# Kernel optimization log

Measured on AMD Instinct MI355X. Metric: run time of the kernel, lower is better.

The kernel has to match this reference:

```python
import jax, jax.numpy as jnp
import numpy as np

N = 50000
E = 1600000
DX = 128
DH = 128
DY = 64
NEG_SLOPE = 0.0  # in_neg_slope; LeakyReLU slope in GAT attention


def _init(key, shape, fan_in):
    return jax.random.normal(key, shape, dtype=jnp.float32) / np.sqrt(fan_in)


def setup_inputs() -> dict:
    key = jax.random.key(0)
    ks = jax.random.split(key, 12)
    node_x = jax.random.normal(ks[0], (N, DX), dtype=jnp.float32)
    edge_index = jax.random.randint(ks[1], (2, E), 0, N, dtype=jnp.int32)
    return {
        "node_x": node_x,
        "edge_index": edge_index,
        # GATConv layer 1 (DX -> DH, heads=1)
        "W1": _init(ks[2], (DX, DH), DX),
        "att_src1": _init(ks[3], (DH,), DH),
        "att_dst1": _init(ks[4], (DH,), DH),
        "b1": jnp.zeros((DH,), dtype=jnp.float32),
        # GATConv layer 2 (DH -> DH)
        "W2": _init(ks[5], (DH, DH), DH),
        "att_src2": _init(ks[6], (DH,), DH),
        "att_dst2": _init(ks[7], (DH,), DH),
        "b2": jnp.zeros((DH,), dtype=jnp.float32),
        # output Linear (DH -> DY)
        "W_out": _init(ks[8], (DH, DY), DH),
        "b_out": jnp.zeros((DY,), dtype=jnp.float32),
    }


def _gat_conv(x, src, dst, W, att_src, att_dst, bias, n):
    # h: [N, DH] transformed features
    h = x @ W
    # per-edge attention logits: a_src . h_j + a_dst . h_i
    e = (h @ att_src)[src] + (h @ att_dst)[dst]          # [E']
    e = jnp.where(e > 0, e, NEG_SLOPE * e)               # LeakyReLU
    # segment softmax over incoming edges of each destination node
    m = jax.lax.stop_gradient(jax.ops.segment_max(e, dst, num_segments=n))
    ex = jnp.exp(e - m[dst])
    denom = jax.ops.segment_sum(ex, dst, num_segments=n)
    alpha = ex / denom[dst]                              # [E']
    # scatter-add weighted source features to destinations
    out = jax.ops.segment_sum(h[src] * alpha[:, None], dst, num_segments=n)
    return out + bias


def reference(node_x, edge_index, W1, att_src1, att_dst1, b1,
              W2, att_src2, att_dst2, b2, W_out, b_out):
    n = node_x.shape[0]
    src, dst = edge_index[0], edge_index[1]
    # PyG GATConv default add_self_loops=True
    loop = jnp.arange(n, dtype=src.dtype)
    src = jnp.concatenate([src, loop])
    dst = jnp.concatenate([dst, loop])
    x1 = jax.nn.relu(_gat_conv(node_x, src, dst, W1, att_src1, att_dst1, b1, n))
    x2 = _gat_conv(x1, src, dst, W2, att_src2, att_dst2, b2, n)
    return x2 @ W_out + b_out
```

## Files before the change

### kernel.cpp

```cpp
#include <hip/hip_runtime.h>
#include <hip/hip_fp16.h>

typedef unsigned short u16;
typedef unsigned int   u32;
typedef _Float16 f16;
typedef __attribute__((ext_vector_type(8))) f16 f16x8;
typedef __attribute__((ext_vector_type(2))) f16 h2;
typedef __attribute__((ext_vector_type(4))) float f32x4;

#define NN 50000
#define EE 1600000
#define DD 128
#define DYY 64
#define NB 196
#define EPB 8192
#define GB 196
#define MAXD 160
#define NTILE 3125
#define GMM 782
#define XST 144

__device__ __forceinline__ u16 f2h(float f){
  union { f16 h; u16 u; } x; x.h = (f16)f; return x.u;
}
__device__ __forceinline__ float wave_sum(float v){
  #pragma unroll
  for (int s = 32; s; s >>= 1) v += __shfl_xor(v, s, 64);
  return v;
}

__device__ __forceinline__ void wfrag_one(const float* __restrict__ W, u16* __restrict__ Wf,
                                          int nct, int s){
  int lane = s & 63;
  int t  = (s >> 6) % nct;
  int ks = (s >> 6) / nct;
  int q = lane >> 4, n = lane & 15;
  int N = nct * 16;
  u16 tmp[8];
  #pragma unroll
  for (int j = 0; j < 8; ++j)
    tmp[j] = f2h(W[(ks * 32 + q * 8 + j) * N + t * 16 + n]);
  *(uint4*)(Wf + (size_t)s * 8) = *(const uint4*)tmp;
}

__global__ __launch_bounds__(256) void kA_prep(const int* __restrict__ dst, int* __restrict__ hist2d,
                                               const float* __restrict__ W1, const float* __restrict__ W2,
                                               const float* __restrict__ Wo,
                                               u16* __restrict__ Wf1, u16* __restrict__ Wf2,
                                               u16* __restrict__ Wfo){
  int b = blockIdx.x, tid = threadIdx.x;
  if (b < GB){
    __shared__ int hist[256];
    hist[tid] = 0;
    __syncthreads();
    int e0 = b * EPB, e1 = min(e0 + EPB, EE);
    for (int e = e0 + tid; e < e1; e += 256) atomicAdd(&hist[dst[e] >> 8], 1);
    __syncthreads();
    hist2d[b * 256 + tid] = hist[tid];
  } else if (b < 204) wfrag_one(W1, Wf1, 8, (b - 196) * 256 + tid);
  else if (b < 212)   wfrag_one(W2, Wf2, 8, (b - 204) * 256 + tid);
  else                wfrag_one(Wo, Wfo, 4, (b - 212) * 256 + tid);
}

__device__ __forceinline__ void gemm_tile(const float* __restrict__ X,
                                          const u16* __restrict__ Wf, u16* __restrict__ Hout,
                                          const float* __restrict__ as, const float* __restrict__ ad,
                                          float* __restrict__ Sv, float* __restrict__ Dv,
                                          int blk, int tid, uint4* Wl){
  const uint4* Wg = (const uint4*)Wf;
  #pragma unroll
  for (int i = 0; i < 8; ++i) Wl[tid + 256 * i] = Wg[tid + 256 * i];
  __syncthreads();
  int wv = tid >> 6, lane = tid & 63;
  int rtile = blk * 4 + wv;
  if (rtile >= NTILE) return;
  int q = lane >> 4, n = lane & 15;
  int arow = rtile * 16 + n;
  f32x4 acc[8];
  #pragma unroll
  for (int t = 0; t < 8; ++t) acc[t] = (f32x4){0.f, 0.f, 0.f, 0.f};
  union F8 { uint4 u; f16x8 v; f16 h[8]; };
  #pragma unroll
  for (int ks = 0; ks < 4; ++ks){
    int kb = ks * 32 + q * 8;
    const float* xp = X + (size_t)arow * DD + kb;
    float4 f0 = *(const float4*)xp;
    float4 f1 = *(const float4*)(xp + 4);
    F8 a;
    a.h[0] = (f16)f0.x; a.h[1] = (f16)f0.y; a.h[2] = (f16)f0.z; a.h[3] = (f16)f0.w;
    a.h[4] = (f16)f1.x; a.h[5] = (f16)f1.y; a.h[6] = (f16)f1.z; a.h[7] = (f16)f1.w;
    #pragma unroll
    for (int t = 0; t < 8; ++t){
      F8 b; b.u = Wl[(ks * 8 + t) * 64 + lane];
      acc[t] = __builtin_amdgcn_mfma_f32_16x16x32_f16(a.v, b.v, acc[t], 0, 0, 0);
    }
  }
  float ps[4] = {0, 0, 0, 0}, pd[4] = {0, 0, 0, 0};
  #pragma unroll
  for (int t = 0; t < 8; ++t){
    float a_s = as[t * 16 + n];
    float a_d = ad[t * 16 + n];
    #pragma unroll
    for (int rg = 0; rg < 4; ++rg){
      ps[rg] += acc[t][rg] * a_s;
      pd[rg] += acc[t][rg] * a_d;
    }
  }
  #pragma unroll
  for (int rg = 0; rg < 4; ++rg){
    #pragma unroll
    for (int s = 1; s < 16; s <<= 1){
      ps[rg] += __shfl_xor(ps[rg], s, 64);
      pd[rg] += __shfl_xor(pd[rg], s, 64);
    }
  }
  #pragma unroll
  for (int rg = 0; rg < 4; ++rg){
    int grow = rtile * 16 + q * 4 + rg;
    if (n == 0){ Sv[grow] = ps[rg]; Dv[grow] = pd[rg]; }
    #pragma unroll
    for (int t = 0; t < 8; ++t)
      Hout[(size_t)grow * DD + t * 16 + n] = f2h(acc[t][rg]);
  }
}

__global__ __launch_bounds__(256) void kBC(const int* __restrict__ src, const int* __restrict__ dst,
                                           const int* __restrict__ hist2d,
                                           int* __restrict__ btot, int* __restrict__ bbase,
                                           u32* __restrict__ buf,
                                           const float* __restrict__ X0, const u16* __restrict__ Wf1,
                                           u16* __restrict__ Hbf1,
                                           const float* __restrict__ as1, const float* __restrict__ ad1,
                                           float* __restrict__ Sv1, float* __restrict__ Dv1){
  __shared__ __align__(16) uint4 Wl[2048];
  int b = blockIdx.x, tid = threadIdx.x;
  if (b < GB){
    int* lcur = (int*)Wl;
    int* sd   = ((int*)Wl) + 256;
    int c = b;
    int pre = 0, tot = 0;
    for (int cc = 0; cc < GB; ++cc){
      int v = hist2d[cc * 256 + tid];
      if (cc < c) pre += v;
      tot += v;
    }
    sd[tid] = tot;
    __syncthreads();
    for (int o = 1; o < 256; o <<= 1){
      int t = (tid >= o) ? sd[tid - o] : 0;
      __syncthreads();
      sd[tid] += t;
      __syncthreads();
    }
    int bb = sd[tid] - tot;
    if (c == 0){ btot[tid] = tot; bbase[tid] = bb; }
    lcur[tid] = bb + pre;
    __syncthreads();
    int e0 = c * EPB, e1 = min(e0 + EPB, EE);
    for (int e = e0 + tid; e < e1; e += 256){
      int d = dst[e];
      int pos = atomicAdd(&lcur[d >> 8], 1);
      buf[pos] = (u32)src[e] | ((u32)(d & 255) << 16);
    }
  } else {
    gemm_tile(X0, Wf1, Hbf1, as1, ad1, Sv1, Dv1, b - GB, tid, Wl);
  }
}

__global__ __launch_bounds__(256) void kD_finalize(const u32* __restrict__ buf,
                                                   const int* __restrict__ btot, const int* __restrict__ bbase,
                                                   int* __restrict__ offs, int* __restrict__ cnt,
                                                   u16* __restrict__ srcs){
  __shared__ int dh[256];
  __shared__ int sd[256];
  __shared__ int dcur[256];
  int tid = threadIdx.x, b = blockIdx.x;
  int n = btot[b], base = bbase[b];
  dh[tid] = 0;
  __syncthreads();
  for (int i = tid; i < n; i += 256) atomicAdd(&dh[(buf[base + i] >> 16) & 255], 1);
  __syncthreads();
  int v = dh[tid];
  sd[tid] = v;
  __syncthreads();
  for (int o = 1; o < 256; o <<= 1){
    int t = (tid >= o) ? sd[tid - o] : 0;
    __syncthreads();
    sd[tid] += t;
    __syncthreads();
  }
  int excl = sd[tid] - v;
  dcur[tid] = base + excl;
  int d = (b << 8) + tid;
  if (d < NN){ offs[d] = base + excl; cnt[d] = v; }
  __syncthreads();
  for (int i = tid; i < n; i += 256){
    u32 u = buf[base + i];
    int pos = atomicAdd(&dcur[(u >> 16) & 255], 1);
    srcs[pos] = (u16)(u & 0xffffu);
  }
}

__device__ void agg_node_lds(const u16* __restrict__ H, const float* __restrict__ Sv,
                             const float* __restrict__ Dv, const int* __restrict__ offs,
                             const int* __restrict__ cnt, const u16* __restrict__ srcs,
                             const float* __restrict__ bias, u16* __restrict__ xrow,
                             int do_relu, int wid, int lane, int* si, float* sw){
  int off = offs[wid], c = cnt[wid];
  float dvw = Dv[wid];
  float wself = __expf(fmaxf(Sv[wid] + dvw, 0.f));
  int cf = min(c, MAXD);
  int grp = lane >> 4, cg_ = lane & 15;
  const u32* H32 = (const u32*)H;
  union F8 { uint4 u; h2 p[4]; };
  F8 rself; rself.u = (uint4){0, 0, 0, 0};
  if (grp == 0) rself.u = *(const uint4*)(H32 + (size_t)wid * 64 + cg_ * 4);
  float dl = 0.f;
  for (int j = lane; j < c; j += 64){
    int sidx = (int)srcs[off + j];
    float wgt = __expf(fmaxf(Sv[sidx] + dvw, 0.f));
    if (j < MAXD){ si[j] = sidx; sw[j] = wgt; }
    dl += wgt;
  }
  float inv = 1.f / (wave_sum(dl) + wself);
  h2 accA[4] = {(h2){0,0},(h2){0,0},(h2){0,0},(h2){0,0}};
  h2 accB[4] = {(h2){0,0},(h2){0,0},(h2){0,0},(h2){0,0}};
  if (grp == 0){
    f16 wh = (f16)(wself * inv); h2 w2 = {wh, wh};
    #pragma unroll
    for (int i = 0; i < 4; ++i) accA[i] = rself.p[i] * w2;
  }
  int base = 0;
  int nfull = cf & ~7;
  for (; base < nfull; base += 8){
    int j0 = base + grp, j1 = j0 + 4;
    int s0 = si[j0], s1 = si[j1];
    float w0 = sw[j0] * inv, w1 = sw[j1] * inv;
    F8 r0; r0.u = *(const uint4*)(H32 + (size_t)s0 * 64 + cg_ * 4);
    F8 r1; r1.u = *(const uint4*)(H32 + (size_t)s1 * 64 + cg_ * 4);
    f16 wh0 = (f16)w0; h2 w20 = {wh0, wh0};
    f16 wh1 = (f16)w1; h2 w21 = {wh1, wh1};
    #pragma unroll
    for (int i = 0; i < 4; ++i){
      accA[i] += r0.p[i] * w20;
      accB[i] += r1.p[i] * w21;
    }
  }
  for (; base < cf; base += 4){
    int j = base + grp;
    float wgt = 0.f; int sidx = 0;
    if (j < cf){ wgt = sw[j] * inv; sidx = si[j]; }
    f16 wh = (f16)wgt; h2 w2 = {wh, wh};
    F8 r; r.u = *(const uint4*)(H32 + (size_t)sidx * 64 + cg_ * 4);
    #pragma unroll
    for (int i = 0; i < 4; ++i) accA[i] += r.p[i] * w2;
  }
  for (int base2 = MAXD; base2 < c; base2 += 4){
    int j = base2 + grp;
    bool valid = j < c;
    int sidx = valid ? (int)srcs[off + j] : 0;
    float wgt = valid ? __expf(fmaxf(Sv[sidx] + dvw, 0.f)) * inv : 0.f;
    f16 wh = (f16)wgt; h2 w2 = {wh, wh};
    F8 r; r.u = *(const uint4*)(H32 + (size_t)sidx * 64 + cg_ * 4);
    #pragma unroll
    for (int i = 0; i < 4; ++i) accA[i] += r.p[i] * w2;
  }
  #pragma unroll
  for (int i = 0; i < 4; ++i) accA[i] += accB[i];
  union FU { h2 v; float f; };
  #pragma unroll
  for (int i = 0; i < 4; ++i){
    FU a; a.v = accA[i];
    FU o1; o1.f = __shfl_xor(a.f, 16, 64); a.v = a.v + o1.v;
    FU o2; o2.f = __shfl_xor(a.f, 32, 64); a.v = a.v + o2.v;
    accA[i] = a.v;
  }
  if (grp == 0){
    uint4 pk;
    u32* pkp = (u32*)&pk;
    #pragma unroll
    for (int qq = 0; qq < 4; ++qq){
      float o0 = (float)accA[qq].x + bias[cg_ * 8 + 2 * qq];
      float o1 = (float)accA[qq].y + bias[cg_ * 8 + 2 * qq + 1];
      if (do_relu){ o0 = fmaxf(o0, 0.f); o1 = fmaxf(o1, 0.f); }
      pkp[qq] = ((u32)f2h(o1) << 16) | (u32)f2h(o0);
    }
    *(uint4*)(xrow + cg_ * 8) = pk;
  }
}

__global__ __launch_bounds__(256, 8) void kE(const u16* __restrict__ Hbf1,
                                          const float* __restrict__ Sv1, const float* __restrict__ Dv1,
                                          const int* __restrict__ offs, const int* __restrict__ cnt,
                                          const u16* __restrict__ srcs, const float* __restrict__ b1,
                                          const u16* __restrict__ Wf2,
                                          const float* __restrict__ as2, const float* __restrict__ ad2,
                                          u16* __restrict__ Hbf2,
                                          float* __restrict__ Sv2, float* __restrict__ Dv2){
  __shared__ __align__(16) u16 Xs[16 * XST];
  __shared__ int   s_i[4][MAXD];
  __shared__ float s_w[4][MAXD];
  __shared__ float svp[16], dvp[16];
  int tid = threadIdx.x, wv = tid >> 6, lane = tid & 63;
  int rtile = blockIdx.x;
  if (tid < 16){ svp[tid] = 0.f; dvp[tid] = 0.f; }
  #pragma unroll
  for (int k = 0; k < 4; ++k){
    int r = wv * 4 + k;
    agg_node_lds(Hbf1, Sv1, Dv1, offs, cnt, srcs, b1, Xs + r * XST, 1,
                 rtile * 16 + r, lane, s_i[wv], s_w[wv]);
  }
  __syncthreads();
  const uint4* Wg = (const uint4*)Wf2;
  int q = lane >> 4, n = lane & 15;
  f32x4 acc[2] = {(f32x4){0.f,0.f,0.f,0.f}, (f32x4){0.f,0.f,0.f,0.f}};
  union F8 { uint4 u; f16x8 v; };
  #pragma unroll
  for (int ks = 0; ks < 4; ++ks){
    F8 a; a.u = *(const uint4*)((const char*)Xs + n * (XST * 2) + ks * 64 + q * 16);
    #pragma unroll
    for (int tt = 0; tt < 2; ++tt){
      F8 b; b.u = Wg[(ks * 8 + wv * 2 + tt) * 64 + lane];
      acc[tt] = __builtin_amdgcn_mfma_f32_16x16x32_f16(a.v, b.v, acc[tt], 0, 0, 0);
    }
  }
  float ps[4] = {0, 0, 0, 0}, pd[4] = {0, 0, 0, 0};
  #pragma unroll
  for (int tt = 0; tt < 2; ++tt){
    int t = wv * 2 + tt;
    float a_s = as2[t * 16 + n];
    float a_d = ad2[t * 16 + n];
    #pragma unroll
    for (int rg = 0; rg < 4; ++rg){
      ps[rg] += acc[tt][rg] * a_s;
      pd[rg] += acc[tt][rg] * a_d;
    }
  }
  #pragma unroll
  for (int rg = 0; rg < 4; ++rg){
    #pragma unroll
    for (int s = 1; s < 16; s <<= 1){
      ps[rg] += __shfl_xor(ps[rg], s, 64);
      pd[rg] += __shfl_xor(pd[rg], s, 64);
    }
  }
  if (n == 0){
    #pragma unroll
    for (int rg = 0; rg < 4; ++rg){
      atomicAdd(&svp[q * 4 + rg], ps[rg]);
      atomicAdd(&dvp[q * 4 + rg], pd[rg]);
    }
  }
  #pragma unroll
  for (int rg = 0; rg < 4; ++rg){
    int grow = rtile * 16 + q * 4 + rg;
    #pragma unroll
    for (int tt = 0; tt < 2; ++tt)
      Hbf2[(size_t)grow * DD + (wv * 2 + tt) * 16 + n] = f2h(acc[tt][rg]);
  }
  __syncthreads();
  if (tid < 16){ Sv2[rtile * 16 + tid] = svp[tid]; Dv2[rtile * 16 + tid] = dvp[tid]; }
}

__global__ __launch_bounds__(256, 8) void kF(const u16* __restrict__ Hbf2,
                                          const float* __restrict__ Sv2, const float* __restrict__ Dv2,
                                          const int* __restrict__ offs, const int* __restrict__ cnt,
                                          const u16* __restrict__ srcs, const float* __restrict__ b2,
                                          const u16* __restrict__ Wfo, const float* __restrict__ bo,
                                          float* __restrict__ out){
  __shared__ __align__(16) u16 Xs[16 * XST];
  __shared__ int   s_i[4][MAXD];
  __shared__ float s_w[4][MAXD];
  int tid = threadIdx.x, wv = tid >> 6, lane = tid & 63;
  int rtile = blockIdx.x;
  #pragma unroll
  for (int k = 0; k < 4; ++k){
    int r = wv * 4 + k;
    agg_node_lds(Hbf2, Sv2, Dv2, offs, cnt, srcs, b2, Xs + r * XST, 0,
                 rtile * 16 + r, lane, s_i[wv], s_w[wv]);
  }
  __syncthreads();
  const uint4* Wg = (const uint4*)Wfo;
  int q = lane >> 4, n = lane & 15;
  f32x4 acc = (f32x4){0.f, 0.f, 0.f, 0.f};
  union F8 { uint4 u; f16x8 v; };
  #pragma unroll
  for (int ks = 0; ks < 4; ++ks){
    F8 a; a.u = *(const uint4*)((const char*)Xs + n * (XST * 2) + ks * 64 + q * 16);
    F8 b; b.u = Wg[(ks * 4 + wv) * 64 + lane];
    acc = __builtin_amdgcn_mfma_f32_16x16x32_f16(a.v, b.v, acc, 0, 0, 0);
  }
  float bt = bo[wv * 16 + n];
  #pragma unroll
  for (int rg = 0; rg < 4; ++rg){
    int grow = rtile * 16 + q * 4 + rg;
    out[(size_t)grow * DYY + wv * 16 + n] = acc[rg] + bt;
  }
}

extern "C" void kernel_launch(void* const* d_in, const int* in_sizes, int n_in,
                              void* d_out, int out_size, void* d_ws, size_t ws_size,
                              hipStream_t stream) {
  const float* node_x = (const float*)d_in[0];
  const int* ei   = (const int*)d_in[1];
  const int* srcp = ei;
  const int* dstp = ei + EE;
  const float* W1  = (const float*)d_in[2];
  const float* as1 = (const float*)d_in[3];
  const float* ad1 = (const float*)d_in[4];
  const float* b1  = (const float*)d_in[5];
  const float* W2  = (const float*)d_in[6];
  const float* as2 = (const float*)d_in[7];
  const float* ad2 = (const float*)d_in[8];
  const float* b2  = (const float*)d_in[9];
  const float* Wo  = (const float*)d_in[10];
  const float* bo  = (const float*)d_in[11];

  char* w = (char*)d_ws;
  u16*   Hbf1  = (u16*)w;  w += (size_t)NN * DD * 2;
  u16*   Hbf2  = (u16*)w;  w += (size_t)NN * DD * 2;
  u32*   buf   = (u32*)Hbf2;
  float* Sv1   = (float*)w; w += (size_t)NN * 4;
  float* Dv1   = (float*)w; w += (size_t)NN * 4;
  float* Sv2   = (float*)w; w += (size_t)NN * 4;
  float* Dv2   = (float*)w; w += (size_t)NN * 4;
  int*   cnt   = (int*)w;   w += (size_t)NN * 4;
  int*   offs  = (int*)w;   w += (size_t)NN * 4;
  int*   btot  = (int*)w;   w += 1024;
  int*   bbase = (int*)w;   w += 1024;
  int*   hist2d = (int*)w;  w += GB * 256 * 4;
  u16*   srcs  = (u16*)w;   w += (size_t)EE * 2;
  u16*   Wf1   = (u16*)w;   w += 32768;
  u16*   Wf2   = (u16*)w;   w += 32768;
  u16*   Wfo   = (u16*)w;   w += 16384;

  const int TB = 256;

  kA_prep    <<<216,      TB, 0, stream>>>(dstp, hist2d, W1, W2, Wo, Wf1, Wf2, Wfo);
  kBC        <<<GB + GMM, TB, 0, stream>>>(srcp, dstp, hist2d, btot, bbase, buf,
                                           node_x, Wf1, Hbf1, as1, ad1, Sv1, Dv1);
  kD_finalize<<<NB,       TB, 0, stream>>>(buf, btot, bbase, offs, cnt, srcs);
  kE         <<<NTILE,    TB, 0, stream>>>(Hbf1, Sv1, Dv1, offs, cnt, srcs, b1,
                                           Wf2, as2, ad2, Hbf2, Sv2, Dv2);
  kF         <<<NTILE,    TB, 0, stream>>>(Hbf2, Sv2, Dv2, offs, cnt, srcs, b2,
                                           Wfo, bo, (float*)d_out);
}
```

Before: 261.1 us.

## Batch softmax prep for four nodes per wave and software-pipeline neighbor row gathers

The per-node aggregation helper is replaced by one that handles four destination nodes per wave together. It loads the edge offsets, counts, source indices and attention weights for all four up front and runs their four wave-sum reductions interleaved, so the dependent latency chains overlap. The gather loop now double-buffers neighbor feature rows, prefetching the next round's two rows while the current round is accumulated. The LDS staging per node shrinks to 64 edges; neighbors beyond 64 take the slower path that re-reads indices and recomputes weights from global memory, which costs more for high-degree nodes.

```diff
diff --git a/kernel.cpp b/kernel.cpp
--- a/kernel.cpp
+++ b/kernel.cpp
@@ -15,18 +15,12 @@
 #define NB 196
 #define EPB 8192
 #define GB 196
-#define MAXD 160
 #define NTILE 3125
 #define GMM 782
 #define XST 144
 
 __device__ __forceinline__ u16 f2h(float f){
   union { f16 h; u16 u; } x; x.h = (f16)f; return x.u;
-}
-__device__ __forceinline__ float wave_sum(float v){
-  #pragma unroll
-  for (int s = 32; s; s >>= 1) v += __shfl_xor(v, s, 64);
-  return v;
 }
 
 __device__ __forceinline__ void wfrag_one(const float* __restrict__ W, u16* __restrict__ Wf,
@@ -201,91 +195,130 @@
   }
 }
 
-__device__ void agg_node_lds(const u16* __restrict__ H, const float* __restrict__ Sv,
-                             const float* __restrict__ Dv, const int* __restrict__ offs,
-                             const int* __restrict__ cnt, const u16* __restrict__ srcs,
-                             const float* __restrict__ bias, u16* __restrict__ xrow,
-                             int do_relu, int wid, int lane, int* si, float* sw){
-  int off = offs[wid], c = cnt[wid];
-  float dvw = Dv[wid];
-  float wself = __expf(fmaxf(Sv[wid] + dvw, 0.f));
-  int cf = min(c, MAXD);
+__device__ void agg4(const u16* __restrict__ H, const float* __restrict__ Sv,
+                     const float* __restrict__ Dv, const int* __restrict__ offs,
+                     const int* __restrict__ cnt, const u16* __restrict__ srcs,
+                     const float* __restrict__ bias, u16* __restrict__ xb,
+                     int do_relu, int wid0, int lane, int* __restrict__ si,
+                     float* __restrict__ sw){
   int grp = lane >> 4, cg_ = lane & 15;
   const u32* H32 = (const u32*)H;
+  int off[4], c[4];
+  float dvw[4], inv[4], invw[4];
+  #pragma unroll
+  for (int k = 0; k < 4; ++k){ off[k] = offs[wid0 + k]; c[k] = cnt[wid0 + k]; }
+  #pragma unroll
+  for (int k = 0; k < 4; ++k) dvw[k] = Dv[wid0 + k];
+  int sreg[4];
+  #pragma unroll
+  for (int k = 0; k < 4; ++k)
+    sreg[k] = (lane < c[k]) ? (int)srcs[off[k] + lane] : 0;
+  float wreg[4], dl[4];
+  #pragma unroll
+  for (int k = 0; k < 4; ++k){
+    float w = (lane < c[k]) ? __expf(fmaxf(Sv[sreg[k]] + dvw[k], 0.f)) : 0.f;
+    wreg[k] = w; dl[k] = w;
+  }
+  #pragma unroll
+  for (int k = 0; k < 4; ++k){
+    for (int j = lane + 64; j < c[k]; j += 64)
+      dl[k] += __expf(fmaxf(Sv[(int)srcs[off[k] + j]] + dvw[k], 0.f));
+  }
+  #pragma unroll
+  for (int k = 0; k < 4; ++k){
+    if (lane < min(c[k], 64)){ si[k * 64 + lane] = sreg[k]; sw[k * 64 + lane] = wreg[k]; }
+  }
+  #pragma unroll
+  for (int s = 32; s; s >>= 1){
+    #pragma unroll
+    for (int k = 0; k < 4; ++k) dl[k] += __shfl_xor(dl[k], s, 64);
+  }
+  #pragma unroll
+  for (int k = 0; k < 4; ++k){
+    float ws = __expf(fmaxf(Sv[wid0 + k] + dvw[k], 0.f));
+    float iv = 1.f / (dl[k] + ws);
+    inv[k] = iv; invw[k] = ws * iv;
+  }
   union F8 { uint4 u; h2 p[4]; };
-  F8 rself; rself.u = (uint4){0, 0, 0, 0};
-  if (grp == 0) rself.u = *(const uint4*)(H32 + (size_t)wid * 64 + cg_ * 4);
-  float dl = 0.f;
-  for (int j = lane; j < c; j += 64){
-    int sidx = (int)srcs[off + j];
-    float wgt = __expf(fmaxf(Sv[sidx] + dvw, 0.f));
-    if (j < MAXD){ si[j] = sidx; sw[j] = wgt; }
-    dl += wgt;
-  }
-  float inv = 1.f / (wave_sum(dl) + wself);
-  h2 accA[4] = {(h2){0,0},(h2){0,0},(h2){0,0},(h2){0,0}};
-  h2 accB[4] = {(h2){0,0},(h2){0,0},(h2){0,0},(h2){0,0}};
-  if (grp == 0){
-    f16 wh = (f16)(wself * inv); h2 w2 = {wh, wh};
-    #pragma unroll
-    for (int i = 0; i < 4; ++i) accA[i] = rself.p[i] * w2;
-  }
-  int base = 0;
-  int nfull = cf & ~7;
-  for (; base < nfull; base += 8){
-    int j0 = base + grp, j1 = j0 + 4;
-    int s0 = si[j0], s1 = si[j1];
-    float w0 = sw[j0] * inv, w1 = sw[j1] * inv;
-    F8 r0; r0.u = *(const uint4*)(H32 + (size_t)s0 * 64 + cg_ * 4);
-    F8 r1; r1.u = *(const uint4*)(H32 + (size_t)s1 * 64 + cg_ * 4);
-    f16 wh0 = (f16)w0; h2 w20 = {wh0, wh0};
-    f16 wh1 = (f16)w1; h2 w21 = {wh1, wh1};
+  #pragma unroll
+  for (int k = 0; k < 4; ++k){
+    int wid = wid0 + k;
+    int cf = min(c[k], 64);
+    const int*   sik = si + k * 64;
+    const float* swk = sw + k * 64;
+    h2 accA[4] = {(h2){0,0},(h2){0,0},(h2){0,0},(h2){0,0}};
+    h2 accB[4] = {(h2){0,0},(h2){0,0},(h2){0,0},(h2){0,0}};
+    F8 rs; rs.u = (uint4){0, 0, 0, 0};
+    if (grp == 0) rs.u = *(const uint4*)(H32 + (size_t)wid * 64 + cg_ * 4);
+    int rounds = (cf + 7) >> 3;
+    uint4 a0 = (uint4){0,0,0,0}, a1 = a0;
+    float w0 = 0.f, w1 = 0.f;
+    if (rounds > 0){
+      int j0 = grp, j1 = grp + 4;
+      int s0 = 0, s1 = 0;
+      if (j0 < cf){ s0 = sik[j0]; w0 = swk[j0]; }
+      if (j1 < cf){ s1 = sik[j1]; w1 = swk[j1]; }
+      a0 = *(const uint4*)(H32 + (size_t)s0 * 64 + cg_ * 4);
+      a1 = *(const uint4*)(H32 + (size_t)s1 * 64 + cg_ * 4);
+    }
+    if (grp == 0){
+      f16 wh = (f16)invw[k]; h2 w2 = {wh, wh};
+      #pragma unroll
+      for (int i = 0; i < 4; ++i) accA[i] = rs.p[i] * w2;
+    }
+    for (int r = 0; r < rounds; ++r){
+      uint4 b0 = (uint4){0,0,0,0}, b1 = b0;
+      float v0 = 0.f, v1 = 0.f;
+      if (r + 1 < rounds){
+        int j0 = (r + 1) * 8 + grp, j1 = j0 + 4;
+        int s0 = 0, s1 = 0;
+        if (j0 < cf){ s0 = sik[j0]; v0 = swk[j0]; }
+        if (j1 < cf){ s1 = sik[j1]; v1 = swk[j1]; }
+        b0 = *(const uint4*)(H32 + (size_t)s0 * 64 + cg_ * 4);
+        b1 = *(const uint4*)(H32 + (size_t)s1 * 64 + cg_ * 4);
+      }
+      F8 r0, r1; r0.u = a0; r1.u = a1;
+      f16 h0 = (f16)(w0 * inv[k]); h2 x0 = {h0, h0};
+      f16 h1 = (f16)(w1 * inv[k]); h2 x1 = {h1, h1};
+      #pragma unroll
+      for (int i = 0; i < 4; ++i){
+        accA[i] += r0.p[i] * x0;
+        accB[i] += r1.p[i] * x1;
+      }
+      a0 = b0; a1 = b1; w0 = v0; w1 = v1;
+    }
+    for (int b2 = 64; b2 < c[k]; b2 += 4){
+      int j = b2 + grp;
+      bool valid = j < c[k];
+      int sidx = valid ? (int)srcs[off[k] + j] : 0;
+      float wgt = valid ? __expf(fmaxf(Sv[sidx] + dvw[k], 0.f)) * inv[k] : 0.f;
+      F8 r; r.u = *(const uint4*)(H32 + (size_t)sidx * 64 + cg_ * 4);
+      f16 wh = (f16)wgt; h2 w2 = {wh, wh};
+      #pragma unroll
+      for (int i = 0; i < 4; ++i) accA[i] += r.p[i] * w2;
+    }
+    #pragma unroll
+    for (int i = 0; i < 4; ++i) accA[i] += accB[i];
+    union FU { h2 v; float f; };
     #pragma unroll
     for (int i = 0; i < 4; ++i){
-      accA[i] += r0.p[i] * w20;
-      accB[i] += r1.p[i] * w21;
-    }
-  }
-  for (; base < cf; base += 4){
-    int j = base + grp;
-    float wgt = 0.f; int sidx = 0;
-    if (j < cf){ wgt = sw[j] * inv; sidx = si[j]; }
-    f16 wh = (f16)wgt; h2 w2 = {wh, wh};
-    F8 r; r.u = *(const uint4*)(H32 + (size_t)sidx * 64 + cg_ * 4);
-    #pragma unroll
-    for (int i = 0; i < 4; ++i) accA[i] += r.p[i] * w2;
-  }
-  for (int base2 = MAXD; base2 < c; base2 += 4){
-    int j = base2 + grp;
-    bool valid = j < c;
-    int sidx = valid ? (int)srcs[off + j] : 0;
-    float wgt = valid ? __expf(fmaxf(Sv[sidx] + dvw, 0.f)) * inv : 0.f;
-    f16 wh = (f16)wgt; h2 w2 = {wh, wh};
-    F8 r; r.u = *(const uint4*)(H32 + (size_t)sidx * 64 + cg_ * 4);
-    #pragma unroll
-    for (int i = 0; i < 4; ++i) accA[i] += r.p[i] * w2;
-  }
-  #pragma unroll
-  for (int i = 0; i < 4; ++i) accA[i] += accB[i];
-  union FU { h2 v; float f; };
-  #pragma unroll
-  for (int i = 0; i < 4; ++i){
-    FU a; a.v = accA[i];
-    FU o1; o1.f = __shfl_xor(a.f, 16, 64); a.v = a.v + o1.v;
-    FU o2; o2.f = __shfl_xor(a.f, 32, 64); a.v = a.v + o2.v;
-    accA[i] = a.v;
-  }
-  if (grp == 0){
-    uint4 pk;
-    u32* pkp = (u32*)&pk;
-    #pragma unroll
-    for (int qq = 0; qq < 4; ++qq){
-      float o0 = (float)accA[qq].x + bias[cg_ * 8 + 2 * qq];
-      float o1 = (float)accA[qq].y + bias[cg_ * 8 + 2 * qq + 1];
-      if (do_relu){ o0 = fmaxf(o0, 0.f); o1 = fmaxf(o1, 0.f); }
-      pkp[qq] = ((u32)f2h(o1) << 16) | (u32)f2h(o0);
-    }
-    *(uint4*)(xrow + cg_ * 8) = pk;
+      FU a; a.v = accA[i];
+      FU o1; o1.f = __shfl_xor(a.f, 16, 64); a.v = a.v + o1.v;
+      FU o2; o2.f = __shfl_xor(a.f, 32, 64); a.v = a.v + o2.v;
+      accA[i] = a.v;
+    }
+    if (grp == 0){
+      uint4 pk;
+      u32* pkp = (u32*)&pk;
+      #pragma unroll
+      for (int qq = 0; qq < 4; ++qq){
+        float o0 = (float)accA[qq].x + bias[cg_ * 8 + 2 * qq];
+        float o1 = (float)accA[qq].y + bias[cg_ * 8 + 2 * qq + 1];
+        if (do_relu){ o0 = fmaxf(o0, 0.f); o1 = fmaxf(o1, 0.f); }
+        pkp[qq] = ((u32)f2h(o1) << 16) | (u32)f2h(o0);
+      }
+      *(uint4*)(xb + k * XST + cg_ * 8) = pk;
+    }
   }
 }
 
@@ -298,18 +331,14 @@
                                           u16* __restrict__ Hbf2,
                                           float* __restrict__ Sv2, float* __restrict__ Dv2){
   __shared__ __align__(16) u16 Xs[16 * XST];
-  __shared__ int   s_i[4][MAXD];
-  __shared__ float s_w[4][MAXD];
+  __shared__ int   s_i[4][4][64];
+  __shared__ float s_w[4][4][64];
   __shared__ float svp[16], dvp[16];
   int tid = threadIdx.x, wv = tid >> 6, lane = tid & 63;
   int rtile = blockIdx.x;
   if (tid < 16){ svp[tid] = 0.f; dvp[tid] = 0.f; }
-  #pragma unroll
-  for (int k = 0; k < 4; ++k){
-    int r = wv * 4 + k;
-    agg_node_lds(Hbf1, Sv1, Dv1, offs, cnt, srcs, b1, Xs + r * XST, 1,
-                 rtile * 16 + r, lane, s_i[wv], s_w[wv]);
-  }
+  agg4(Hbf1, Sv1, Dv1, offs, cnt, srcs, b1, Xs + (wv * 4) * XST, 1,
+       rtile * 16 + wv * 4, lane, &s_i[wv][0][0], &s_w[wv][0][0]);
   __syncthreads();
   const uint4* Wg = (const uint4*)Wf2;
   int q = lane >> 4, n = lane & 15;
@@ -369,16 +398,12 @@
                                           const u16* __restrict__ Wfo, const float* __restrict__ bo,
                                           float* __restrict__ out){
   __shared__ __align__(16) u16 Xs[16 * XST];
-  __shared__ int   s_i[4][MAXD];
-  __shared__ float s_w[4][MAXD];
+  __shared__ int   s_i[4][4][64];
+  __shared__ float s_w[4][4][64];
   int tid = threadIdx.x, wv = tid >> 6, lane = tid & 63;
   int rtile = blockIdx.x;
-  #pragma unroll
-  for (int k = 0; k < 4; ++k){
-    int r = wv * 4 + k;
-    agg_node_lds(Hbf2, Sv2, Dv2, offs, cnt, srcs, b2, Xs + r * XST, 0,
-                 rtile * 16 + r, lane, s_i[wv], s_w[wv]);
-  }
+  agg4(Hbf2, Sv2, Dv2, offs, cnt, srcs, b2, Xs + (wv * 4) * XST, 0,
+       rtile * 16 + wv * 4, lane, &s_i[wv][0][0], &s_w[wv][0][0]);
   __syncthreads();
   const uint4* Wg = (const uint4*)Wfo;
   int q = lane >> 4, n = lane & 15;
```

Result: slower. 348.8 us (+33.6%).

## Apply output projection before layer-2 aggregation to gather 64-wide rows

Applied to the files above, without the earlier changes.

Because aggregation is linear and the softmax weights sum to one, the output Linear is moved ahead of layer-2 neighbor aggregation. kE now computes G2 = H2·W_out per node, and kF gathers 64-wide fp16 rows instead of 128-wide ones, adding a precomputed constant b2·W_out + b_out. This halves the gather traffic in the last aggregation and removes the final MFMA from kF. The cost is an extra small GEMM plus LDS round trip in kE, and a different fp16 rounding order.

```diff
diff --git a/kernel.cpp b/kernel.cpp
--- a/kernel.cpp
+++ b/kernel.cpp
@@ -46,8 +46,9 @@
 __global__ __launch_bounds__(256) void kA_prep(const int* __restrict__ dst, int* __restrict__ hist2d,
                                                const float* __restrict__ W1, const float* __restrict__ W2,
                                                const float* __restrict__ Wo,
+                                               const float* __restrict__ b2, const float* __restrict__ bo,
                                                u16* __restrict__ Wf1, u16* __restrict__ Wf2,
-                                               u16* __restrict__ Wfo){
+                                               u16* __restrict__ Wfo, float* __restrict__ c64){
   int b = blockIdx.x, tid = threadIdx.x;
   if (b < GB){
     __shared__ int hist[256];
@@ -59,7 +60,12 @@
     hist2d[b * 256 + tid] = hist[tid];
   } else if (b < 204) wfrag_one(W1, Wf1, 8, (b - 196) * 256 + tid);
   else if (b < 212)   wfrag_one(W2, Wf2, 8, (b - 204) * 256 + tid);
-  else                wfrag_one(Wo, Wfo, 4, (b - 212) * 256 + tid);
+  else if (b < 216)   wfrag_one(Wo, Wfo, 4, (b - 212) * 256 + tid);
+  else if (tid < DYY){
+    float s = bo[tid];
+    for (int k = 0; k < DD; ++k) s += b2[k] * Wo[k * DYY + tid];
+    c64[tid] = s;
+  }
 }
 
 __device__ __forceinline__ void gemm_tile(const float* __restrict__ X,
@@ -293,9 +299,9 @@
                                           const float* __restrict__ Sv1, const float* __restrict__ Dv1,
                                           const int* __restrict__ offs, const int* __restrict__ cnt,
                                           const u16* __restrict__ srcs, const float* __restrict__ b1,
-                                          const u16* __restrict__ Wf2,
+                                          const u16* __restrict__ Wf2, const u16* __restrict__ Wfo,
                                           const float* __restrict__ as2, const float* __restrict__ ad2,
-                                          u16* __restrict__ Hbf2,
+                                          u16* __restrict__ G2,
                                           float* __restrict__ Sv2, float* __restrict__ Dv2){
   __shared__ __align__(16) u16 Xs[16 * XST];
   __shared__ int   s_i[4][MAXD];
@@ -351,51 +357,121 @@
       atomicAdd(&dvp[q * 4 + rg], pd[rg]);
     }
   }
+  __syncthreads();
+  if (tid < 16){ Sv2[rtile * 16 + tid] = svp[tid]; Dv2[rtile * 16 + tid] = dvp[tid]; }
+  #pragma unroll
+  for (int tt = 0; tt < 2; ++tt)
+    #pragma unroll
+    for (int rg = 0; rg < 4; ++rg)
+      Xs[(q * 4 + rg) * XST + (wv * 2 + tt) * 16 + n] = f2h(acc[tt][rg]);
+  __syncthreads();
+  const uint4* Wo4 = (const uint4*)Wfo;
+  f32x4 g = (f32x4){0.f, 0.f, 0.f, 0.f};
+  #pragma unroll
+  for (int ks = 0; ks < 4; ++ks){
+    F8 a; a.u = *(const uint4*)((const char*)Xs + n * (XST * 2) + ks * 64 + q * 16);
+    F8 b; b.u = Wo4[(ks * 4 + wv) * 64 + lane];
+    g = __builtin_amdgcn_mfma_f32_16x16x32_f16(a.v, b.v, g, 0, 0, 0);
+  }
   #pragma unroll
   for (int rg = 0; rg < 4; ++rg){
     int grow = rtile * 16 + q * 4 + rg;
-    #pragma unroll
-    for (int tt = 0; tt < 2; ++tt)
-      Hbf2[(size_t)grow * DD + (wv * 2 + tt) * 16 + n] = f2h(acc[tt][rg]);
-  }
-  __syncthreads();
-  if (tid < 16){ Sv2[rtile * 16 + tid] = svp[tid]; Dv2[rtile * 16 + tid] = dvp[tid]; }
-}
-
-__global__ __launch_bounds__(256, 8) void kF(const u16* __restrict__ Hbf2,
+    G2[(size_t)grow * DYY + wv * 16 + n] = f2h(g[rg]);
+  }
+}
+
+__device__ void agg_node_out(const u16* __restrict__ G2v, const float* __restrict__ Sv,
+                             const float* __restrict__ Dv, const int* __restrict__ offs,
+                             const int* __restrict__ cnt, const u16* __restrict__ srcs,
+                             const float* __restrict__ c64, float* __restrict__ out,
+                             int wid, int lane, int* si, float* sw){
+  int off = offs[wid], c = cnt[wid];
+  float dvw = Dv[wid];
+  float wself = __expf(fmaxf(Sv[wid] + dvw, 0.f));
+  int cf = min(c, MAXD);
+  int grp = lane >> 4, cg_ = lane & 15;
+  const u32* G = (const u32*)G2v;
+  union F4 { uint2 u; h2 p[2]; };
+  F4 rself; rself.u = (uint2){0, 0};
+  if (grp == 0) rself.u = *(const uint2*)(G + (size_t)wid * 32 + cg_ * 2);
+  float dl = 0.f;
+  for (int j = lane; j < c; j += 64){
+    int sidx = (int)srcs[off + j];
+    float wgt = __expf(fmaxf(Sv[sidx] + dvw, 0.f));
+    if (j < MAXD){ si[j] = sidx; sw[j] = wgt; }
+    dl += wgt;
+  }
+  float inv = 1.f / (wave_sum(dl) + wself);
+  h2 accA[2] = {(h2){0,0},(h2){0,0}};
+  h2 accB[2] = {(h2){0,0},(h2){0,0}};
+  if (grp == 0){
+    f16 wh = (f16)(wself * inv); h2 w2 = {wh, wh};
+    accA[0] = rself.p[0] * w2; accA[1] = rself.p[1] * w2;
+  }
+  int base = 0;
+  int nfull = cf & ~7;
+  for (; base < nfull; base += 8){
+    int j0 = base + grp, j1 = j0 + 4;
+    int s0 = si[j0], s1 = si[j1];
+    float w0 = sw[j0] * inv, w1 = sw[j1] * inv;
+    F4 r0; r0.u = *(const uint2*)(G + (size_t)s0 * 32 + cg_ * 2);
+    F4 r1; r1.u = *(const uint2*)(G + (size_t)s1 * 32 + cg_ * 2);
+    f16 wh0 = (f16)w0; h2 x0 = {wh0, wh0};
+    f16 wh1 = (f16)w1; h2 x1 = {wh1, wh1};
+    accA[0] += r0.p[0] * x0; accA[1] += r0.p[1] * x0;
+    accB[0] += r1.p[0] * x1; accB[1] += r1.p[1] * x1;
+  }
+  for (; base < cf; base += 4){
+    int j = base + grp;
+    float wgt = 0.f; int sidx = 0;
+    if (j < cf){ wgt = sw[j] * inv; sidx = si[j]; }
+    f16 wh = (f16)wgt; h2 w2 = {wh, wh};
+    F4 r; r.u = *(const uint2*)(G + (size_t)sidx * 32 + cg_ * 2);
+    accA[0] += r.p[0] * w2; accA[1] += r.p[1] * w2;
+  }
+  for (int b2i = MAXD; b2i < c; b2i += 4){
+    int j = b2i + grp;
+    bool valid = j < c;
+    int sidx = valid ? (int)srcs[off + j] : 0;
+    float wgt = valid ? __expf(fmaxf(Sv[sidx] + dvw, 0.f)) * inv : 0.f;
+    F4 r; r.u = *(const uint2*)(G + (size_t)sidx * 32 + cg_ * 2);
+    f16 wh = (f16)wgt; h2 w2 = {wh, wh};
+    accA[0] += r.p[0] * w2; accA[1] += r.p[1] * w2;
+  }
+  accA[0] += accB[0]; accA[1] += accB[1];
+  union FU { h2 v; float f; };
+  #pragma unroll
+  for (int i = 0; i < 2; ++i){
+    FU a; a.v = accA[i];
+    FU o1; o1.f = __shfl_xor(a.f, 16, 64); a.v = a.v + o1.v;
+    FU o2; o2.f = __shfl_xor(a.f, 32, 64); a.v = a.v + o2.v;
+    accA[i] = a.v;
+  }
+  if (grp == 0){
+    float4 cv = *(const float4*)(c64 + cg_ * 4);
+    float4 o;
+    o.x = (float)accA[0].x + cv.x;
+    o.y = (float)accA[0].y + cv.y;
+    o.z = (float)accA[1].x + cv.z;
+    o.w = (float)accA[1].y + cv.w;
+    *(float4*)(out + (size_t)wid * DYY + cg_ * 4) = o;
+  }
+}
+
+__global__ __launch_bounds__(256, 8) void kF(const u16* __restrict__ G2,
                                           const float* __restrict__ Sv2, const float* __restrict__ Dv2,
                                           const int* __restrict__ offs, const int* __restrict__ cnt,
-                                          const u16* __restrict__ srcs, const float* __restrict__ b2,
-                                          const u16* __restrict__ Wfo, const float* __restrict__ bo,
+                                          const u16* __restrict__ srcs,
+                                          const float* __restrict__ c64,
                                           float* __restrict__ out){
-  __shared__ __align__(16) u16 Xs[16 * XST];
   __shared__ int   s_i[4][MAXD];
   __shared__ float s_w[4][MAXD];
   int tid = threadIdx.x, wv = tid >> 6, lane = tid & 63;
   int rtile = blockIdx.x;
   #pragma unroll
-  for (int k = 0; k < 4; ++k){
-    int r = wv * 4 + k;
-    agg_node_lds(Hbf2, Sv2, Dv2, offs, cnt, srcs, b2, Xs + r * XST, 0,
-                 rtile * 16 + r, lane, s_i[wv], s_w[wv]);
-  }
-  __syncthreads();
-  const uint4* Wg = (const uint4*)Wfo;
-  int q = lane >> 4, n = lane & 15;
-  f32x4 acc = (f32x4){0.f, 0.f, 0.f, 0.f};
-  union F8 { uint4 u; f16x8 v; };
-  #pragma unroll
-  for (int ks = 0; ks < 4; ++ks){
-    F8 a; a.u = *(const uint4*)((const char*)Xs + n * (XST * 2) + ks * 64 + q * 16);
-    F8 b; b.u = Wg[(ks * 4 + wv) * 64 + lane];
-    acc = __builtin_amdgcn_mfma_f32_16x16x32_f16(a.v, b.v, acc, 0, 0, 0);
-  }
-  float bt = bo[wv * 16 + n];
-  #pragma unroll
-  for (int rg = 0; rg < 4; ++rg){
-    int grow = rtile * 16 + q * 4 + rg;
-    out[(size_t)grow * DYY + wv * 16 + n] = acc[rg] + bt;
-  }
+  for (int k = 0; k < 4; ++k)
+    agg_node_out(G2, Sv2, Dv2, offs, cnt, srcs, c64, out,
+                 rtile * 16 + wv * 4 + k, lane, s_i[wv], s_w[wv]);
 }
 
 extern "C" void kernel_launch(void* const* d_in, const int* in_sizes, int n_in,
@@ -418,8 +494,8 @@
 
   char* w = (char*)d_ws;
   u16*   Hbf1  = (u16*)w;  w += (size_t)NN * DD * 2;
-  u16*   Hbf2  = (u16*)w;  w += (size_t)NN * DD * 2;
-  u32*   buf   = (u32*)Hbf2;
+  u32*   buf   = (u32*)w;
+  u16*   G2    = (u16*)w;  w += (size_t)EE * 4;
   float* Sv1   = (float*)w; w += (size_t)NN * 4;
   float* Dv1   = (float*)w; w += (size_t)NN * 4;
   float* Sv2   = (float*)w; w += (size_t)NN * 4;
@@ -433,15 +509,17 @@
   u16*   Wf1   = (u16*)w;   w += 32768;
   u16*   Wf2   = (u16*)w;   w += 32768;
   u16*   Wfo   = (u16*)w;   w += 16384;
+  float* c64   = (float*)w; w += 256;
 
   const int TB = 256;
 
-  kA_prep    <<<216,      TB, 0, stream>>>(dstp, hist2d, W1, W2, Wo, Wf1, Wf2, Wfo);
+  kA_prep    <<<217,      TB, 0, stream>>>(dstp, hist2d, W1, W2, Wo, b2, bo,
+                                           Wf1, Wf2, Wfo, c64);
   kBC        <<<GB + GMM, TB, 0, stream>>>(srcp, dstp, hist2d, btot, bbase, buf,
                                            node_x, Wf1, Hbf1, as1, ad1, Sv1, Dv1);
   kD_finalize<<<NB,       TB, 0, stream>>>(buf, btot, bbase, offs, cnt, srcs);
   kE         <<<NTILE,    TB, 0, stream>>>(Hbf1, Sv1, Dv1, offs, cnt, srcs, b1,
-                                           Wf2, as2, ad2, Hbf2, Sv2, Dv2);
-  kF         <<<NTILE,    TB, 0, stream>>>(Hbf2, Sv2, Dv2, offs, cnt, srcs, b2,
-                                           Wfo, bo, (float*)d_out);
-}
+                                           Wf2, Wfo, as2, ad2, G2, Sv2, Dv2);
+  kF         <<<NTILE,    TB, 0, stream>>>(G2, Sv2, Dv2, offs, cnt, srcs, c64,
+                                           (float*)d_out);
+}
```

Result: faster. 245.5 us (-6.0%).
